# Performance work log

Hardware: AMD Instinct MI355X
Metric: run time of the kernel (lower is better)

## Reference

```python
import jax, jax.numpy as jnp
import numpy as np


def _conv(x, w, b, pad):
    # NCHW conv, stride 1, symmetric padding, torch Conv2d semantics (bias included)
    y = jax.lax.conv_general_dilated(x, w, (1, 1), [(pad, pad), (pad, pad)],
                                     dimension_numbers=('NCHW', 'OIHW', 'NCHW'))
    return y + b[None, :, None, None]


def _inorm(x, eps=1e-5):
    # torch nn.InstanceNorm2d default: affine=False, biased variance over (H, W)
    m = jnp.mean(x, axis=(2, 3), keepdims=True)
    v = jnp.var(x, axis=(2, 3), keepdims=True)
    return (x - m) * jax.lax.rsqrt(v + eps)


def _convT2x(x, wt):
    # torch ConvTranspose2d(k=3, stride=2, padding=1, output_padding=1, bias=False)
    # wt has torch layout (C_in, C_out, kH, kW); express as dilated conv with flipped kernel.
    # output size = 2*H exactly: pad low = k-1-p = 1, pad high = k-1-p+output_padding = 2.
    w = jnp.transpose(jnp.flip(wt, (2, 3)), (1, 0, 2, 3))  # -> (C_out, C_in, kH, kW)
    return jax.lax.conv_general_dilated(x, w, (1, 1), [(1, 2), (1, 2)],
                                        lhs_dilation=(2, 2),
                                        dimension_numbers=('NCHW', 'OIHW', 'NCHW'))


def setup_inputs() -> dict:
    key = jax.random.key(0)
    ks = jax.random.split(key, 24)
    B, C = 2, 256          # dim_list[0] = 256
    H4, W4 = 160, 240      # 1/4-scale feature map of a 640x960 image

    def n(k, shape, s=1.0):
        return jax.random.normal(k, shape, dtype=jnp.float32) * s

    return {
        # mono feature pyramid: 1/4, 1/8, 1/16, 1/32 scale, all C=dim_list[0]
        'f4':  n(ks[0], (B, C, H4, W4)),
        'f8':  n(ks[1], (B, C, H4 // 2, W4 // 2)),
        'f16': n(ks[2], (B, C, H4 // 4, W4 // 4)),
        'f32': n(ks[3], (B, C, H4 // 8, W4 // 8)),
        'w32': n(ks[4], (160, C, 3, 3), 0.02), 'b32': n(ks[5], (160,), 0.02),
        'wt32': n(ks[6], (160, 192, 3, 3), 0.02),
        'w16': n(ks[7], (192, 192 + C, 5, 5), 0.02), 'b16': n(ks[8], (192,), 0.02),
        'wr16': n(ks[9], (192, C, 1, 1), 0.02), 'br16': n(ks[10], (192,), 0.02),
        'wt16': n(ks[11], (192, 64, 3, 3), 0.02),
        'w8': n(ks[12], (64, 64 + C, 5, 5), 0.02), 'b8': n(ks[13], (64,), 0.02),
        'wr8': n(ks[14], (64, C, 1, 1), 0.02), 'br8': n(ks[15], (64,), 0.02),
        'wt8': n(ks[16], (64, 48, 3, 3), 0.02),
        'w4': n(ks[17], (48, 48 + C, 5, 5), 0.02), 'b4': n(ks[18], (48,), 0.02),
        'wr4': n(ks[19], (48, C, 1, 1), 0.02), 'br4': n(ks[20], (48,), 0.02),
    }


def reference(f4, f8, f16, f32, w32, b32, wt32, w16, b16, wr16, br16, wt16,
              w8, b8, wr8, br8, wt8, w4, b4, wr4, br4):
    # Feat_transfer.forward: coarse-to-fine fusion with residual 1x1 projections
    feat32 = jax.nn.relu(_inorm(_conv(f32, w32, b32, 1)))                 # [B,160,H/32,W/32]
    up32 = _convT2x(feat32, wt32)                                          # [B,192,H/16,W/16]
    feat16 = jax.nn.relu(_inorm(_conv(jnp.concatenate([f16, up32], 1), w16, b16, 2))) \
             + _conv(f16, wr16, br16, 0)                                   # [B,192,H/16,W/16]
    up16 = _convT2x(feat16, wt16)                                          # [B,64,H/8,W/8]
    feat8 = jax.nn.relu(_inorm(_conv(jnp.concatenate([f8, up16], 1), w8, b8, 2))) \
            + _conv(f8, wr8, br8, 0)                                       # [B,64,H/8,W/8]
    up8 = _convT2x(feat8, wt8)                                             # [B,48,H/4,W/4]
    feat4 = jax.nn.relu(_inorm(_conv(jnp.concatenate([f4, up8], 1), w4, b4, 2))) \
            + _conv(f4, wr4, br4, 0)                                       # [B,48,H/4,W/4]
    return (feat4, feat8, feat16, feat32)
```

## Files before the change

kernel.cpp:

```cpp
#include <hip/hip_runtime.h>
#include <hip/hip_bf16.h>

typedef __attribute__((ext_vector_type(8))) short bf16x8;
typedef __attribute__((ext_vector_type(4))) float f32x4;

static inline int cdiv(int a, int b) { return (a + b - 1) / b; }

__device__ __forceinline__ ushort f2bf(float f) {
    unsigned u = __float_as_uint(f);
    unsigned r = (u + 0x7FFFu + ((u >> 16) & 1u)) >> 16;
    return (ushort)r;
}
__device__ __forceinline__ unsigned pack2bf(float lo, float hi) {
    unsigned r;
    asm("v_cvt_pk_bf16_f32 %0, %1, %2" : "=v"(r) : "v"(lo), "v"(hi));
    return r;
}
__device__ __forceinline__ float bf2f(ushort u) {
    return __uint_as_float((unsigned)u << 16);
}

__global__ __launch_bounds__(256)
void transpose_w(const float* __restrict__ w, ushort* __restrict__ wt,
                 int Cout, int CoutPad, int Cin, int Cin_pad, int KK, int total) {
    int idx = blockIdx.x * 256 + threadIdx.x;
    if (idx >= total) return;
    int ci = idx % Cin_pad;
    int rem = idx / Cin_pad;
    int co = rem % CoutPad;
    int t  = rem / CoutPad;
    float v = (ci < Cin && co < Cout) ? w[((size_t)co * Cin + ci) * KK + t] : 0.f;
    wt[idx] = f2bf(v);
}

__device__ const int g_tky[9] = {1, 1, 1, 0, 2, 0, 0, 2, 2};
__device__ const int g_tkx[9] = {1, 0, 2, 1, 1, 0, 2, 0, 2};

__global__ __launch_bounds__(256)
void transpose_wt(const float* __restrict__ wt, ushort* __restrict__ dst,
                  int Cin, int Cout, int Cin_pad, int total) {
    int idx = blockIdx.x * 256 + threadIdx.x;
    if (idx >= total) return;
    int ci = idx % Cin_pad;
    int rem = idx / Cin_pad;
    int co = rem % Cout;
    int t  = rem / Cout;
    float v = 0.f;
    if (ci < Cin)
        v = wt[((size_t)(ci * Cout + co) * 3 + g_tky[t]) * 3 + g_tkx[t]];
    dst[idx] = f2bf(v);
}

template<int K, int TY, int TX, int NSPLIT, int MSPLIT, int MT, int OUTMODE>
__global__ __launch_bounds__(256)
void conv_mfma7(const float* __restrict__ in1, int C1,
                const ushort* __restrict__ in2, int C2, int Cin,
                const ushort* __restrict__ wt,
                void* __restrict__ outDst, size_t pStride,
                int H, int W, int Cout, int CoutPad, int Cin_pad,
                int tilesX, int tilesY, int nchunks, int cps) {
    constexpr int P = K / 2;
    constexpr int XOFF = (K == 1) ? 0 : 4;
    constexpr int JOFF = XOFF - P;
    constexpr int HXs = (TX + K - 1 + JOFF + 3) & ~3;
    constexpr int HY = TY + K - 1;
    constexpr int PITCH = 40;
    constexpr int KK = K * K;
    constexpr int PXW = TY * TX / NSPLIT;
    constexpr int NT = PXW / 16;
    constexpr int G = HXs / 4;
    constexpr int NITEM = 16 * HY * G;

    __shared__ ushort sT[HY * HXs * PITCH];

    const int tid = threadIdx.x;
    const int lane = tid & 63, wv = tid >> 6;
    const int nwave = wv % NSPLIT, mwave = wv / NSPLIT;
    const int l15 = lane & 15, lg = lane >> 4;

    const int nwg = tilesX * tilesY;
    int bid = blockIdx.x;
    int q8 = nwg >> 3, r8 = nwg & 7;
    int xcd = bid & 7, sidx = bid >> 3;
    int wg = (xcd < r8 ? xcd * (q8 + 1) : r8 * (q8 + 1) + (xcd - r8) * q8) + sidx;
    const int txi = wg / tilesY;
    const int tyi = wg % tilesY;

    const int b = blockIdx.z;
    const int x0 = txi * TX, y0 = tyi * TY;
    const size_t HW = (size_t)H * W;

    const int co0 = mwave * (MT * 16);

    int posBase[NT], py_[NT], px_[NT];
    #pragma unroll
    for (int nt = 0; nt < NT; ++nt) {
        int pidx = nwave * PXW + nt * 16 + l15;
        int py = pidx / TX, px = pidx % TX;
        py_[nt] = py; px_[nt] = px;
        posBase[nt] = (py * HXs + px + JOFF) * PITCH + lg * 8;
    }
    const int aoff = l15 * Cin_pad + lg * 8;

    f32x4 acc[MT][NT];
    #pragma unroll
    for (int i = 0; i < MT; ++i)
        #pragma unroll
        for (int j = 0; j < NT; ++j) acc[i][j] = (f32x4)0.f;

    const int c0 = blockIdx.y * cps;
    const int c1 = (c0 + cps < nchunks) ? c0 + cps : nchunks;

    for (int c = c0; c < c1; ++c) {
        const int ci0 = c * 32;
        __syncthreads();
        for (int i = tid; i < NITEM; i += 256) {
            int g  = i % G;
            int rr = (i / G) % HY;
            int cp = i / (G * HY);
            int ci = ci0 + cp * 2;
            int y  = y0 - P + rr;
            int xg = x0 - XOFF + g * 4;
            ushort* dp = &sT[(rr * HXs + g * 4) * PITCH + cp * 2];
            bool yok = (unsigned)y < (unsigned)H;
            unsigned d0, d1, d2, d3;
            if (ci < C1) {
                const float* p0 = in1 + (long long)(b * C1 + ci) * (long long)HW + (long long)y * W + xg;
                if (yok && xg >= 0 && (xg + 3) < W) {
                    float4 a  = *(const float4*)p0;
                    float4 b2 = *(const float4*)(p0 + HW);
                    d0 = pack2bf(a.x, b2.x);
                    d1 = pack2bf(a.y, b2.y);
                    d2 = pack2bf(a.z, b2.z);
                    d3 = pack2bf(a.w, b2.w);
                } else {
                    unsigned t0 = 0, t1 = 0, t2 = 0, t3 = 0;
                    #pragma unroll
                    for (int u = 0; u < 4; ++u) {
                        int x = xg + u;
                        unsigned pk = 0;
                        if (yok && (unsigned)x < (unsigned)W)
                            pk = (unsigned)f2bf(p0[u]) | ((unsigned)f2bf(p0[u + (long long)HW]) << 16);
                        if (u == 0) t0 = pk; else if (u == 1) t1 = pk;
                        else if (u == 2) t2 = pk; else t3 = pk;
                    }
                    d0 = t0; d1 = t1; d2 = t2; d3 = t3;
                }
            } else {
                const ushort* q0 = in2 + (long long)(b * C2 + (ci - C1)) * (long long)HW + (long long)y * W + xg;
                if (yok && xg >= 0 && (xg + 3) < W && (ci + 1) < Cin) {
                    ushort4 a  = *(const ushort4*)q0;
                    ushort4 b2 = *(const ushort4*)(q0 + HW);
                    d0 = (unsigned)a.x | ((unsigned)b2.x << 16);
                    d1 = (unsigned)a.y | ((unsigned)b2.y << 16);
                    d2 = (unsigned)a.z | ((unsigned)b2.z << 16);
                    d3 = (unsigned)a.w | ((unsigned)b2.w << 16);
                } else {
                    unsigned t0 = 0, t1 = 0, t2 = 0, t3 = 0;
                    #pragma unroll
                    for (int u = 0; u < 4; ++u) {
                        int x = xg + u;
                        unsigned pk = 0;
                        if (yok && (unsigned)x < (unsigned)W && ci < Cin) {
                            unsigned v0 = q0[u];
                            unsigned v1 = (ci + 1 < Cin) ? q0[u + (long long)HW] : 0u;
                            pk = v0 | (v1 << 16);
                        }
                        if (u == 0) t0 = pk; else if (u == 1) t1 = pk;
                        else if (u == 2) t2 = pk; else t3 = pk;
                    }
                    d0 = t0; d1 = t1; d2 = t2; d3 = t3;
                }
            }
            int s = (g + rr) & 3;
            #pragma unroll
            for (int u = 0; u < 4; ++u) {
                int cc2 = (u + s) & 3;
                unsigned val = (cc2 & 2) ? ((cc2 & 1) ? d3 : d2)
                                         : ((cc2 & 1) ? d1 : d0);
                *(unsigned*)(dp + cc2 * PITCH) = val;
            }
        }
        __syncthreads();

        bf16x8 af[4][MT];
        #pragma unroll
        for (int s = 0; s < 3; ++s) {
            if (s < KK) {
                const ushort* ap = wt + (size_t)((size_t)s * CoutPad + co0) * Cin_pad + ci0 + aoff;
                #pragma unroll
                for (int mt = 0; mt < MT; ++mt)
                    af[s][mt] = *(const bf16x8*)(ap + (size_t)mt * 16 * Cin_pad);
            }
        }
        #pragma unroll
        for (int t = 0; t < KK; ++t) {
            if (t + 3 < KK) {
                const ushort* ap = wt + (size_t)((size_t)(t + 3) * CoutPad + co0) * Cin_pad + ci0 + aoff;
                #pragma unroll
                for (int mt = 0; mt < MT; ++mt)
                    af[(t + 3) & 3][mt] = *(const bf16x8*)(ap + (size_t)mt * 16 * Cin_pad);
            }
            const int tOff = ((t / K) * HXs + (t % K)) * PITCH;
            bf16x8 bf[NT];
            #pragma unroll
            for (int nt = 0; nt < NT; ++nt)
                bf[nt] = *(const bf16x8*)(sT + posBase[nt] + tOff);
            #pragma unroll
            for (int mt = 0; mt < MT; ++mt)
                #pragma unroll
                for (int nt = 0; nt < NT; ++nt)
                    acc[mt][nt] = __builtin_amdgcn_mfma_f32_16x16x32_bf16(
                        af[t & 3][mt], bf[nt], acc[mt][nt], 0, 0, 0);
        }
    }

    float* baseF = (float*)outDst + (size_t)blockIdx.y * pStride;
    #pragma unroll
    for (int mt = 0; mt < MT; ++mt) {
        #pragma unroll
        for (int nt = 0; nt < NT; ++nt) {
            int y = y0 + py_[nt], x = x0 + px_[nt];
            if (y < H && x < W) {
                #pragma unroll
                for (int r = 0; r < 4; ++r) {
                    int co = co0 + mt * 16 + lg * 4 + r;
                    if (co < Cout) {
                        size_t o = ((size_t)(b * Cout + co)) * HW + (size_t)y * W + x;
                        if (OUTMODE == 0) baseF[o] = acc[mt][nt][r];
                        else              ((ushort*)outDst)[o] = f2bf(acc[mt][nt][r]);
                    }
                }
            }
        }
    }
}

template<int K, int TY, int TX, int NSPLIT, int MSPLIT, int MT>
__global__ __launch_bounds__(256)
void conv_mfma5(const float* __restrict__ in1, int C1, int Cin,
                const ushort* __restrict__ wt,
                float* __restrict__ outDst,
                int H, int W, int Cout, int CoutPad, int Cin_pad,
                int tilesX, int nchunks, int cps) {
    constexpr int P = K / 2;
    constexpr int XOFF = 4;
    constexpr int JOFF = XOFF - P;
    constexpr int HXs = (TX + K - 1 + JOFF + 3) & ~3;
    constexpr int HY = TY + K - 1;
    constexpr int PITCH = 40;
    constexpr int KK = K * K;
    constexpr int PXW = TY * TX / NSPLIT;
    constexpr int NT = PXW / 16;
    constexpr int G = HXs / 4;
    constexpr int NITEM = 16 * HY * G;

    __shared__ ushort sT[HY * HXs * PITCH];

    const int tid = threadIdx.x;
    const int lane = tid & 63, wv = tid >> 6;
    const int nwave = wv % NSPLIT, mwave = wv / NSPLIT;
    const int l15 = lane & 15, lg = lane >> 4;

    const int txi = blockIdx.x % tilesX;
    const int tyi = blockIdx.x / tilesX;
    const int b = blockIdx.z;
    const int x0 = txi * TX, y0 = tyi * TY;
    const size_t HW = (size_t)H * W;
    const int co0 = mwave * (MT * 16);

    int posBase[NT], py_[NT], px_[NT];
    #pragma unroll
    for (int nt = 0; nt < NT; ++nt) {
        int pidx = nwave * PXW + nt * 16 + l15;
        int py = pidx / TX, px = pidx % TX;
        py_[nt] = py; px_[nt] = px;
        posBase[nt] = (py * HXs + px + JOFF) * PITCH + lg * 8;
    }
    const int aoff = l15 * Cin_pad + lg * 8;

    f32x4 acc[MT][NT];
    #pragma unroll
    for (int i = 0; i < MT; ++i)
        #pragma unroll
        for (int j = 0; j < NT; ++j) acc[i][j] = (f32x4)0.f;

    const int c0 = blockIdx.y * cps;
    const int c1 = (c0 + cps < nchunks) ? c0 + cps : nchunks;

    for (int c = c0; c < c1; ++c) {
        const int ci0 = c * 32;
        __syncthreads();
        for (int i = tid; i < NITEM; i += 256) {
            int g  = i % G;
            int rr = (i / G) % HY;
            int cp = i / (G * HY);
            int ci = ci0 + cp * 2;
            int y  = y0 - P + rr;
            int xg = x0 - XOFF + g * 4;
            ushort* dp = &sT[(rr * HXs + g * 4) * PITCH + cp * 2];
            const float* p0 = in1 + (long long)(b * C1 + ci) * (long long)HW + (long long)y * W + xg;
            bool yok = (unsigned)y < (unsigned)H;
            #pragma unroll
            for (int u = 0; u < 4; ++u) {
                int x = xg + u;
                unsigned pk = 0;
                if (yok && (unsigned)x < (unsigned)W)
                    pk = (unsigned)f2bf(p0[u]) | ((unsigned)f2bf(p0[u + (long long)HW]) << 16);
                *(unsigned*)(dp + u * PITCH) = pk;
            }
        }
        __syncthreads();

        bf16x8 afA[MT];
        {
            const ushort* ap = wt + (size_t)co0 * Cin_pad + ci0 + aoff;
            #pragma unroll
            for (int mt = 0; mt < MT; ++mt)
                afA[mt] = *(const bf16x8*)(ap + (size_t)mt * 16 * Cin_pad);
        }
        #pragma unroll
        for (int t = 0; t < KK; ++t) {
            bf16x8 afB[MT];
            if (t + 1 < KK) {
                const ushort* ap = wt + (size_t)((t + 1) * CoutPad + co0) * Cin_pad + ci0 + aoff;
                #pragma unroll
                for (int mt = 0; mt < MT; ++mt)
                    afB[mt] = *(const bf16x8*)(ap + (size_t)mt * 16 * Cin_pad);
            }
            const int tOff = ((t / K) * HXs + (t % K)) * PITCH;
            bf16x8 bf[NT];
            #pragma unroll
            for (int nt = 0; nt < NT; ++nt)
                bf[nt] = *(const bf16x8*)(sT + posBase[nt] + tOff);
            #pragma unroll
            for (int mt = 0; mt < MT; ++mt)
                #pragma unroll
                for (int nt = 0; nt < NT; ++nt)
                    acc[mt][nt] = __builtin_amdgcn_mfma_f32_16x16x32_bf16(
                        afA[mt], bf[nt], acc[mt][nt], 0, 0, 0);
            if (t + 1 < KK) {
                #pragma unroll
                for (int mt = 0; mt < MT; ++mt) afA[mt] = afB[mt];
            }
        }
    }

    #pragma unroll
    for (int mt = 0; mt < MT; ++mt) {
        #pragma unroll
        for (int nt = 0; nt < NT; ++nt) {
            int y = y0 + py_[nt], x = x0 + px_[nt];
            if (y < H && x < W) {
                #pragma unroll
                for (int r = 0; r < 4; ++r) {
                    int co = co0 + mt * 16 + lg * 4 + r;
                    if (co < Cout) {
                        size_t o = ((size_t)(b * Cout + co)) * HW + (size_t)y * W + x;
                        unsafeAtomicAdd(&outDst[o], acc[mt][nt][r]);
                    }
                }
            }
        }
    }
}

template<int TY, int TX, int NSPLIT, int MT>
__global__ __launch_bounds__(256)
void convt_mfma(const float* __restrict__ in,
                const ushort* __restrict__ wtp,
                ushort* __restrict__ out,
                int Cin, int Cout, int Cin_pad, int Hin, int Win,
                int tilesX, int tilesY) {
    constexpr int HY = TY + 1, HX = TX + 1;
    constexpr int PITCH = 40;
    constexpr int NPX = TY * TX;
    constexpr int PXW = NPX / NSPLIT;
    constexpr int NT = PXW / 16;
    constexpr int NPOS = HY * HX;
    constexpr int NIT = (NPOS * 16 + 63) & ~63;

    __shared__ ushort sT[NPOS * PITCH];

    constexpr int toy[9] = {0, 0, 0, 1, 0, 1, 1, 0, 0};
    constexpr int tox[9] = {0, 1, 0, 0, 0, 1, 0, 1, 0};
    constexpr int tph[9] = {0, 1, 1, 2, 2, 3, 3, 3, 3};

    const int tid = threadIdx.x;
    const int lane = tid & 63, wv = tid >> 6;
    const int nwave = wv % NSPLIT, mwave = wv / NSPLIT;
    const int l15 = lane & 15, lg = lane >> 4;

    int tile = blockIdx.x;
    const int txi = tile % tilesX;
    int rem = tile / tilesX;
    const int tyi = rem % tilesY;
    const int b = rem / tilesY;
    const int x0 = txi * TX, y0 = tyi * TY;
    const size_t HWi = (size_t)Hin * Win;
    const int Wo = 2 * Win;
    const size_t HWo = (size_t)4 * HWi;

    const int co0 = mwave * (MT * 16);

    int posBase[NT], py_[NT], px_[NT];
    #pragma unroll
    for (int nt = 0; nt < NT; ++nt) {
        int pidx = nwave * PXW + nt * 16 + l15;
        int py = pidx / TX, px = pidx % TX;
        py_[nt] = py; px_[nt] = px;
        posBase[nt] = (py * HX + px) * PITCH + lg * 8;
    }
    const int aoff = l15 * Cin_pad + lg * 8;

    f32x4 acc[4][MT][NT];
    #pragma unroll
    for (int p = 0; p < 4; ++p)
        #pragma unroll
        for (int i = 0; i < MT; ++i)
            #pragma unroll
            for (int j = 0; j < NT; ++j) acc[p][i][j] = (f32x4)0.f;

    const int nchunks = Cin_pad / 32;
    for (int c = 0; c < nchunks; ++c) {
        const int ci0 = c * 32;
        __syncthreads();
        for (int i = tid; i < NIT; i += 256) {
            int cp = (i >> 2) & 15;
            int pos = (i & 3) | ((i >> 6) << 2);
            if (pos < NPOS) {
                int hy = pos / HX, hx = pos % HX;
                int y = y0 + hy, x = x0 + hx;
                int ci = ci0 + cp * 2;
                unsigned pk = 0;
                if ((unsigned)y < (unsigned)Hin && (unsigned)x < (unsigned)Win && ci < Cin) {
                    const float* p0 = in + (size_t)(b * Cin + ci) * HWi + (size_t)y * Win + x;
                    float v0 = p0[0];
                    float v1 = (ci + 1 < Cin) ? p0[HWi] : 0.f;
                    pk = pack2bf(v0, v1);
                }
                *(unsigned*)&sT[pos * PITCH + cp * 2] = pk;
            }
        }
        __syncthreads();

        bf16x8 afA[MT];
        {
            const ushort* ap = wtp + (size_t)co0 * Cin_pad + ci0 + aoff;
            #pragma unroll
            for (int mt = 0; mt < MT; ++mt)
                afA[mt] = *(const bf16x8*)(ap + (size_t)mt * 16 * Cin_pad);
        }
        #pragma unroll
        for (int t = 0; t < 9; ++t) {
            bf16x8 afB[MT];
            if (t + 1 < 9) {
                const ushort* ap = wtp + (size_t)((t + 1) * Cout + co0) * Cin_pad + ci0 + aoff;
                #pragma unroll
                for (int mt = 0; mt < MT; ++mt)
                    afB[mt] = *(const bf16x8*)(ap + (size_t)mt * 16 * Cin_pad);
            }
            const int tOff = (toy[t] * HX + tox[t]) * PITCH;
            bf16x8 bf[NT];
            #pragma unroll
            for (int nt = 0; nt < NT; ++nt)
                bf[nt] = *(const bf16x8*)(sT + posBase[nt] + tOff);
            #pragma unroll
            for (int mt = 0; mt < MT; ++mt)
                #pragma unroll
                for (int nt = 0; nt < NT; ++nt)
                    acc[tph[t]][mt][nt] = __builtin_amdgcn_mfma_f32_16x16x32_bf16(
                        afA[mt], bf[nt], acc[tph[t]][mt][nt], 0, 0, 0);
            if (t + 1 < 9) {
                #pragma unroll
                for (int mt = 0; mt < MT; ++mt) afA[mt] = afB[mt];
            }
        }
    }

    #pragma unroll
    for (int dy = 0; dy < 2; ++dy) {
        #pragma unroll
        for (int mt = 0; mt < MT; ++mt) {
            #pragma unroll
            for (int nt = 0; nt < NT; ++nt) {
                int y = y0 + py_[nt], x = x0 + px_[nt];
                if (y < Hin && x < Win) {
                    #pragma unroll
                    for (int r = 0; r < 4; ++r) {
                        int co = co0 + mt * 16 + lg * 4 + r;
                        unsigned pk = pack2bf(acc[dy * 2][mt][nt][r], acc[dy * 2 + 1][mt][nt][r]);
                        *(unsigned*)&out[((size_t)(b * Cout + co)) * HWo + (size_t)(2 * y + dy) * Wo + 2 * x] = pk;
                    }
                }
            }
        }
    }
}

__global__ __launch_bounds__(256)
void inorm_stats2(const float* __restrict__ x, size_t pStride, int NS,
                  float* __restrict__ mean, float* __restrict__ istd, int HW) {
    int bc = blockIdx.x;
    const float4* p = (const float4*)(x + (size_t)bc * HW);
    size_t st4 = pStride >> 2;
    int n4 = HW >> 2;
    float s = 0.f, ss = 0.f;
    for (int i = threadIdx.x; i < n4; i += 256) {
        float4 v = p[i];
        for (int sp = 1; sp < NS; ++sp) {
            float4 w = p[i + sp * st4];
            v.x += w.x; v.y += w.y; v.z += w.z; v.w += w.w;
        }
        s += v.x + v.y + v.z + v.w;
        ss += v.x * v.x + v.y * v.y + v.z * v.z + v.w * v.w;
    }
    #pragma unroll
    for (int o = 32; o > 0; o >>= 1) {
        s  += __shfl_down(s, o);
        ss += __shfl_down(ss, o);
    }
    __shared__ float sh[4][2];
    int wid = threadIdx.x >> 6, ln = threadIdx.x & 63;
    if (ln == 0) { sh[wid][0] = s; sh[wid][1] = ss; }
    __syncthreads();
    if (threadIdx.x == 0) {
        float S = 0.f, SS = 0.f;
        for (int i = 0; i < 4; ++i) { S += sh[i][0]; SS += sh[i][1]; }
        float m = S / HW;
        float v = SS / HW - m * m;
        v = v > 0.f ? v : 0.f;
        mean[bc] = m;
        istd[bc] = rsqrtf(v + 1e-5f);
    }
}

template<int RESMODE>
__global__ __launch_bounds__(256)
void epilogue2(const float* __restrict__ raw, size_t rawStride, int NS,
               const float* __restrict__ mean,
               const float* __restrict__ istd,
               const void* __restrict__ res, size_t resStride, int NSR,
               const float* __restrict__ br,
               float* __restrict__ feat,
               int HW, int Cout, int total4) {
    int i = blockIdx.x * 256 + threadIdx.x;
    if (i >= total4) return;
    int bc = (int)(((long long)i * 4) / HW);
    float m = mean[bc], is = istd[bc];
    size_t rs4 = rawStride >> 2;
    float4 r = ((const float4*)raw)[i];
    for (int sp = 1; sp < NS; ++sp) {
        float4 w = ((const float4*)raw)[i + sp * rs4];
        r.x += w.x; r.y += w.y; r.z += w.z; r.w += w.w;
    }
    float4 o;
    o.x = fmaxf((r.x - m) * is, 0.f);
    o.y = fmaxf((r.y - m) * is, 0.f);
    o.z = fmaxf((r.z - m) * is, 0.f);
    o.w = fmaxf((r.w - m) * is, 0.f);
    if (RESMODE == 1) {
        float bb = br[bc % Cout];
        size_t es4 = resStride >> 2;
        float4 e = ((const float4*)res)[i];
        for (int sp = 1; sp < NSR; ++sp) {
            float4 w = ((const float4*)res)[i + sp * es4];
            e.x += w.x; e.y += w.y; e.z += w.z; e.w += w.w;
        }
        o.x += e.x + bb; o.y += e.y + bb; o.z += e.z + bb; o.w += e.w + bb;
    } else if (RESMODE == 2) {
        float bb = br[bc % Cout];
        ushort4 e = ((const ushort4*)res)[i];
        o.x += bf2f(e.x) + bb; o.y += bf2f(e.y) + bb;
        o.z += bf2f(e.z) + bb; o.w += bf2f(e.w) + bb;
    }
    ((float4*)feat)[i] = o;
}

extern "C" void kernel_launch(void* const* d_in, const int* in_sizes, int n_in,
                              void* d_out, int out_size, void* d_ws, size_t ws_size,
                              hipStream_t stream) {
    const float* f4   = (const float*)d_in[0];
    const float* f8   = (const float*)d_in[1];
    const float* f16  = (const float*)d_in[2];
    const float* f32  = (const float*)d_in[3];
    const float* w32  = (const float*)d_in[4];
    const float* wt32 = (const float*)d_in[6];
    const float* w16  = (const float*)d_in[7];
    const float* wr16 = (const float*)d_in[9];
    const float* br16 = (const float*)d_in[10];
    const float* wt16 = (const float*)d_in[11];
    const float* w8   = (const float*)d_in[12];
    const float* wr8  = (const float*)d_in[14];
    const float* br8  = (const float*)d_in[15];
    const float* wt8  = (const float*)d_in[16];
    const float* w4   = (const float*)d_in[17];
    const float* wr4  = (const float*)d_in[19];
    const float* br4  = (const float*)d_in[20];

    float* out = (float*)d_out;

    const int B = 2, C = 256;
    const int H4 = 160, W4 = 240;
    const int H8 = 80,  W8 = 120;
    const int H16 = 40, W16 = 60;
    const int H32 = 20, W32 = 30;

    float* feat4  = out;
    float* feat8  = out + (size_t)B * 48 * H4 * W4;
    float* feat16 = feat8 + (size_t)B * 64 * H8 * W8;
    float* feat32 = feat16 + (size_t)B * 192 * H16 * W16;

    const size_t bufElems = (size_t)B * 48 * H4 * W4;
    ushort* wsUpB  = (ushort*)d_ws;
    float*  wsRawP = (float*)(wsUpB + bufElems);
    ushort* wsResB = (ushort*)(wsRawP + bufElems);
    float*  stMean = (float*)(wsResB + bufElems);
    float*  stIstd = stMean + 512;
    float*  wsResF = (float*)wsResB;

    ushort* wb = (ushort*)feat4;
    ushort* W32p = wb;
    ushort* W16p = W32p + 9 * 192 * 256;
    ushort* W8p  = W16p + 25 * 192 * 448;
    ushort* W4p  = W8p  + 25 * 64 * 320;
    ushort* R16p = W4p  + 25 * 64 * 320;
    ushort* R8p  = R16p + 192 * 256;
    ushort* R4p  = R8p  + 64 * 256;
    ushort* T32p = R4p  + 64 * 256;
    ushort* T16p = T32p + 9 * 192 * 160;
    ushort* T8p  = T16p + 9 * 64 * 192;

    {
        int t1 = 9 * 192 * 256;
        transpose_w<<<cdiv(t1, 256), 256, 0, stream>>>(w32, W32p, 160, 192, 256, 256, 9, t1);
        int t2 = 25 * 192 * 448;
        transpose_w<<<cdiv(t2, 256), 256, 0, stream>>>(w16, W16p, 192, 192, 448, 448, 25, t2);
        int t3 = 25 * 64 * 320;
        transpose_w<<<cdiv(t3, 256), 256, 0, stream>>>(w8, W8p, 64, 64, 320, 320, 25, t3);
        int t4 = 25 * 64 * 320;
        transpose_w<<<cdiv(t4, 256), 256, 0, stream>>>(w4, W4p, 48, 64, 304, 320, 25, t4);
        int t5 = 192 * 256;
        transpose_w<<<cdiv(t5, 256), 256, 0, stream>>>(wr16, R16p, 192, 192, 256, 256, 1, t5);
        int t6 = 64 * 256;
        transpose_w<<<cdiv(t6, 256), 256, 0, stream>>>(wr8, R8p, 64, 64, 256, 256, 1, t6);
        int t7 = 64 * 256;
        transpose_w<<<cdiv(t7, 256), 256, 0, stream>>>(wr4, R4p, 48, 64, 256, 256, 1, t7);
        int u1 = 9 * 192 * 160;
        transpose_wt<<<cdiv(u1, 256), 256, 0, stream>>>(wt32, T32p, 160, 192, 160, u1);
        int u2 = 9 * 64 * 192;
        transpose_wt<<<cdiv(u2, 256), 256, 0, stream>>>(wt16, T16p, 192, 64, 192, u2);
        int u3 = 9 * 48 * 64;
        transpose_wt<<<cdiv(u3, 256), 256, 0, stream>>>(wt8, T8p, 64, 48, 64, u3);
    }

    {
        hipMemsetAsync(wsRawP, 0, (size_t)B * 160 * H32 * W32 * 4, stream);
        int tX = cdiv(W32, 8), tY = cdiv(H32, 4);
        dim3 g(tX * tY, 8, B);
        conv_mfma5<3, 4, 8, 1, 4, 3><<<g, 256, 0, stream>>>(
            f32, C, C, W32p, wsRawP, H32, W32, 160, 192, 256, tX, 8, 1);
        inorm_stats2<<<B * 160, 256, 0, stream>>>(wsRawP, 0, 1, stMean, stIstd, H32 * W32);
        int tot4 = B * 160 * H32 * W32 / 4;
        epilogue2<0><<<cdiv(tot4, 256), 256, 0, stream>>>(
            wsRawP, 0, 1, stMean, stIstd, nullptr, 0, 0, nullptr, feat32, H32 * W32, 160, tot4);
        int uX = cdiv(W32, 8), uY = cdiv(H32, 2);
        convt_mfma<2, 8, 1, 3><<<uX * uY * B, 256, 0, stream>>>(
            feat32, T32p, wsUpB, 160, 192, 160, H32, W32, uX, uY);
    }
    {
        size_t SZ16 = (size_t)B * 192 * H16 * W16;
        int tX = cdiv(W16, 8), tY = cdiv(H16, 8);
        dim3 g(tX * tY, 4, B);
        conv_mfma7<5, 8, 8, 1, 4, 3, 0><<<g, 256, 0, stream>>>(
            f16, C, wsUpB, 192, 448, W16p, wsRawP, SZ16,
            H16, W16, 192, 192, 448, tX, tY, 14, 4);
        dim3 gr(tX * tY, 2, B);
        conv_mfma7<1, 8, 8, 1, 4, 3, 0><<<gr, 256, 0, stream>>>(
            f16, C, nullptr, 0, C, R16p, wsResF, SZ16,
            H16, W16, 192, 192, 256, tX, tY, 8, 4);
        inorm_stats2<<<B * 192, 256, 0, stream>>>(wsRawP, SZ16, 4, stMean, stIstd, H16 * W16);
        int tot4 = (int)(SZ16 / 4);
        epilogue2<1><<<cdiv(tot4, 256), 256, 0, stream>>>(
            wsRawP, SZ16, 4, stMean, stIstd, wsResF, SZ16, 2, br16, feat16, H16 * W16, 192, tot4);
        int uX = cdiv(W16, 8), uY = cdiv(H16, 4);
        convt_mfma<4, 8, 2, 2><<<uX * uY * B, 256, 0, stream>>>(
            feat16, T16p, wsUpB, 192, 64, 192, H16, W16, uX, uY);
    }
    {
        size_t SZ8 = (size_t)B * 64 * H8 * W8;
        int tX = cdiv(W8, 16), tY = cdiv(H8, 8);
        dim3 g(tX * tY, 3, B);
        conv_mfma7<5, 8, 16, 2, 2, 2, 0><<<g, 256, 0, stream>>>(
            f8, C, wsUpB, 64, 320, W8p, wsRawP, SZ8,
            H8, W8, 64, 64, 320, tX, tY, 10, 4);
        dim3 gr(tX * cdiv(H8, 4), 1, B);
        conv_mfma7<1, 4, 16, 1, 4, 1, 0><<<gr, 256, 0, stream>>>(
            f8, C, nullptr, 0, C, R8p, wsResF, SZ8,
            H8, W8, 64, 64, 256, tX, cdiv(H8, 4), 8, 8);
        inorm_stats2<<<B * 64, 256, 0, stream>>>(wsRawP, SZ8, 3, stMean, stIstd, H8 * W8);
        int tot4 = (int)(SZ8 / 4);
        epilogue2<1><<<cdiv(tot4, 256), 256, 0, stream>>>(
            wsRawP, SZ8, 3, stMean, stIstd, wsResF, SZ8, 1, br8, feat8, H8 * W8, 64, tot4);
        int uX = cdiv(W8, 16), uY = cdiv(H8, 4);
        convt_mfma<4, 16, 4, 3><<<uX * uY * B, 256, 0, stream>>>(
            feat8, T8p, wsUpB, 64, 48, 64, H8, W8, uX, uY);
    }
    {
        size_t SZ4 = (size_t)B * 48 * H4 * W4;
        int tX = cdiv(W4, 16), tY = cdiv(H4, 8);
        dim3 g(tX * tY, 1, B);
        conv_mfma7<5, 8, 16, 2, 2, 2, 0><<<g, 256, 0, stream>>>(
            f4, C, wsUpB, 48, 304, W4p, wsRawP, SZ4,
            H4, W4, 48, 64, 320, tX, tY, 10, 10);
        conv_mfma7<1, 8, 16, 2, 2, 2, 2><<<g, 256, 0, stream>>>(
            f4, C, nullptr, 0, C, R4p, wsResB, 0,
            H4, W4, 48, 64, 256, tX, tY, 8, 8);
        inorm_stats2<<<B * 48, 256, 0, stream>>>(wsRawP, 0, 1, stMean, stIstd, H4 * W4);
        int tot4 = (int)(SZ4 / 4);
        epilogue2<2><<<cdiv(tot4, 256), 256, 0, stream>>>(
            wsRawP, 0, 1, stMean, stIstd, wsResB, 0, 0, br4, feat4, H4 * W4, 48, tot4);
    }
}
```

Before: 594.1 us.

## Raise split-K for 5x5 convs and store bf16 partial sums

The 5x5 fusion convs now split the input-channel reduction across more blocks (7, 5 and 2 splits instead of 4, 3 and 1), and the 1/16 conv uses smaller spatial tiles. To keep the extra partial buffers cheap, each split writes its partial sums as bf16 instead of fp32. New stats and epilogue kernels read and sum the bf16 partials. This adds parallelism and occupancy for the small-resolution convs and cuts partial-sum traffic, at the cost of bf16 rounding on every partial before the instance norm and more partial buffers to read back.

```diff
diff --git a/kernel.cpp b/kernel.cpp
--- a/kernel.cpp
+++ b/kernel.cpp
@@ -215,7 +215,8 @@
         }
     }
 
-    float* baseF = (float*)outDst + (size_t)blockIdx.y * pStride;
+    float*  baseF = (float*)outDst + (size_t)blockIdx.y * pStride;
+    ushort* baseU = (ushort*)outDst + (size_t)blockIdx.y * pStride;
     #pragma unroll
     for (int mt = 0; mt < MT; ++mt) {
         #pragma unroll
@@ -228,7 +229,7 @@
                     if (co < Cout) {
                         size_t o = ((size_t)(b * Cout + co)) * HW + (size_t)y * W + x;
                         if (OUTMODE == 0) baseF[o] = acc[mt][nt][r];
-                        else              ((ushort*)outDst)[o] = f2bf(acc[mt][nt][r]);
+                        else              baseU[o] = f2bf(acc[mt][nt][r]);
                     }
                 }
             }
@@ -535,9 +536,64 @@
     }
 }
 
+__global__ __launch_bounds__(256)
+void inorm_statsB(const ushort* __restrict__ x, size_t pStride, int NS,
+                  float* __restrict__ mean, float* __restrict__ istd, int HW) {
+    int bc = blockIdx.x;
+    const ushort* base = x + (size_t)bc * HW;
+    int n4 = HW >> 2;
+    float s = 0.f, ss = 0.f;
+    for (int i = threadIdx.x; i < n4; i += 256) {
+        float v0 = 0.f, v1 = 0.f, v2 = 0.f, v3 = 0.f;
+        for (int sp = 0; sp < NS; ++sp) {
+            ushort4 u = *(const ushort4*)(base + sp * pStride + (size_t)i * 4);
+            v0 += bf2f(u.x); v1 += bf2f(u.y); v2 += bf2f(u.z); v3 += bf2f(u.w);
+        }
+        s += v0 + v1 + v2 + v3;
+        ss += v0 * v0 + v1 * v1 + v2 * v2 + v3 * v3;
+    }
+    #pragma unroll
+    for (int o = 32; o > 0; o >>= 1) {
+        s  += __shfl_down(s, o);
+        ss += __shfl_down(ss, o);
+    }
+    __shared__ float sh[4][2];
+    int wid = threadIdx.x >> 6, ln = threadIdx.x & 63;
+    if (ln == 0) { sh[wid][0] = s; sh[wid][1] = ss; }
+    __syncthreads();
+    if (threadIdx.x == 0) {
+        float S = 0.f, SS = 0.f;
+        for (int i = 0; i < 4; ++i) { S += sh[i][0]; SS += sh[i][1]; }
+        float m = S / HW;
+        float v = SS / HW - m * m;
+        v = v > 0.f ? v : 0.f;
+        mean[bc] = m;
+        istd[bc] = rsqrtf(v + 1e-5f);
+    }
+}
+
+__global__ __launch_bounds__(256)
+void epilogue2(const float* __restrict__ raw,
+               const float* __restrict__ mean,
+               const float* __restrict__ istd,
+               float* __restrict__ feat,
+               int HW, int total4) {
+    int i = blockIdx.x * 256 + threadIdx.x;
+    if (i >= total4) return;
+    int bc = (int)(((long long)i * 4) / HW);
+    float m = mean[bc], is = istd[bc];
+    float4 r = ((const float4*)raw)[i];
+    float4 o;
+    o.x = fmaxf((r.x - m) * is, 0.f);
+    o.y = fmaxf((r.y - m) * is, 0.f);
+    o.z = fmaxf((r.z - m) * is, 0.f);
+    o.w = fmaxf((r.w - m) * is, 0.f);
+    ((float4*)feat)[i] = o;
+}
+
 template<int RESMODE>
 __global__ __launch_bounds__(256)
-void epilogue2(const float* __restrict__ raw, size_t rawStride, int NS,
+void epilogueB(const ushort* __restrict__ rawB, size_t rawStride, int NS,
                const float* __restrict__ mean,
                const float* __restrict__ istd,
                const void* __restrict__ res, size_t resStride, int NSR,
@@ -548,19 +604,18 @@
     if (i >= total4) return;
     int bc = (int)(((long long)i * 4) / HW);
     float m = mean[bc], is = istd[bc];
-    size_t rs4 = rawStride >> 2;
-    float4 r = ((const float4*)raw)[i];
-    for (int sp = 1; sp < NS; ++sp) {
-        float4 w = ((const float4*)raw)[i + sp * rs4];
-        r.x += w.x; r.y += w.y; r.z += w.z; r.w += w.w;
+    float r0 = 0.f, r1 = 0.f, r2 = 0.f, r3 = 0.f;
+    for (int sp = 0; sp < NS; ++sp) {
+        ushort4 u = *(const ushort4*)(rawB + sp * rawStride + (size_t)i * 4);
+        r0 += bf2f(u.x); r1 += bf2f(u.y); r2 += bf2f(u.z); r3 += bf2f(u.w);
     }
     float4 o;
-    o.x = fmaxf((r.x - m) * is, 0.f);
-    o.y = fmaxf((r.y - m) * is, 0.f);
-    o.z = fmaxf((r.z - m) * is, 0.f);
-    o.w = fmaxf((r.w - m) * is, 0.f);
+    o.x = fmaxf((r0 - m) * is, 0.f);
+    o.y = fmaxf((r1 - m) * is, 0.f);
+    o.z = fmaxf((r2 - m) * is, 0.f);
+    o.w = fmaxf((r3 - m) * is, 0.f);
+    float bb = br[bc % Cout];
     if (RESMODE == 1) {
-        float bb = br[bc % Cout];
         size_t es4 = resStride >> 2;
         float4 e = ((const float4*)res)[i];
         for (int sp = 1; sp < NSR; ++sp) {
@@ -568,8 +623,7 @@
             e.x += w.x; e.y += w.y; e.z += w.z; e.w += w.w;
         }
         o.x += e.x + bb; o.y += e.y + bb; o.z += e.z + bb; o.w += e.w + bb;
-    } else if (RESMODE == 2) {
-        float bb = br[bc % Cout];
+    } else {
         ushort4 e = ((const ushort4*)res)[i];
         o.x += bf2f(e.x) + bb; o.y += bf2f(e.y) + bb;
         o.z += bf2f(e.z) + bb; o.w += bf2f(e.w) + bb;
@@ -613,11 +667,12 @@
 
     const size_t bufElems = (size_t)B * 48 * H4 * W4;
     ushort* wsUpB  = (ushort*)d_ws;
-    float*  wsRawP = (float*)(wsUpB + bufElems);
-    ushort* wsResB = (ushort*)(wsRawP + bufElems);
+    ushort* wsRawB = (ushort*)(wsUpB + bufElems);
+    ushort* wsResB = (ushort*)(wsRawB + 2 * bufElems);
     float*  stMean = (float*)(wsResB + bufElems);
     float*  stIstd = stMean + 512;
     float*  wsResF = (float*)wsResB;
+    float*  wsRawF = (float*)wsRawB;
 
     ushort* wb = (ushort*)feat4;
     ushort* W32p = wb;
@@ -655,34 +710,34 @@
     }
 
     {
-        hipMemsetAsync(wsRawP, 0, (size_t)B * 160 * H32 * W32 * 4, stream);
+        hipMemsetAsync(wsRawF, 0, (size_t)B * 160 * H32 * W32 * 4, stream);
         int tX = cdiv(W32, 8), tY = cdiv(H32, 4);
         dim3 g(tX * tY, 8, B);
         conv_mfma5<3, 4, 8, 1, 4, 3><<<g, 256, 0, stream>>>(
-            f32, C, C, W32p, wsRawP, H32, W32, 160, 192, 256, tX, 8, 1);
-        inorm_stats2<<<B * 160, 256, 0, stream>>>(wsRawP, 0, 1, stMean, stIstd, H32 * W32);
+            f32, C, C, W32p, wsRawF, H32, W32, 160, 192, 256, tX, 8, 1);
+        inorm_stats2<<<B * 160, 256, 0, stream>>>(wsRawF, 0, 1, stMean, stIstd, H32 * W32);
         int tot4 = B * 160 * H32 * W32 / 4;
-        epilogue2<0><<<cdiv(tot4, 256), 256, 0, stream>>>(
-            wsRawP, 0, 1, stMean, stIstd, nullptr, 0, 0, nullptr, feat32, H32 * W32, 160, tot4);
+        epilogue2<<<cdiv(tot4, 256), 256, 0, stream>>>(
+            wsRawF, stMean, stIstd, feat32, H32 * W32, tot4);
         int uX = cdiv(W32, 8), uY = cdiv(H32, 2);
         convt_mfma<2, 8, 1, 3><<<uX * uY * B, 256, 0, stream>>>(
             feat32, T32p, wsUpB, 160, 192, 160, H32, W32, uX, uY);
     }
     {
         size_t SZ16 = (size_t)B * 192 * H16 * W16;
-        int tX = cdiv(W16, 8), tY = cdiv(H16, 8);
-        dim3 g(tX * tY, 4, B);
-        conv_mfma7<5, 8, 8, 1, 4, 3, 0><<<g, 256, 0, stream>>>(
-            f16, C, wsUpB, 192, 448, W16p, wsRawP, SZ16,
-            H16, W16, 192, 192, 448, tX, tY, 14, 4);
+        int tX = cdiv(W16, 8), tY = cdiv(H16, 4);
+        dim3 g(tX * tY, 7, B);
+        conv_mfma7<5, 4, 8, 1, 4, 3, 2><<<g, 256, 0, stream>>>(
+            f16, C, wsUpB, 192, 448, W16p, wsRawB, SZ16,
+            H16, W16, 192, 192, 448, tX, tY, 14, 2);
         dim3 gr(tX * tY, 2, B);
-        conv_mfma7<1, 8, 8, 1, 4, 3, 0><<<gr, 256, 0, stream>>>(
+        conv_mfma7<1, 4, 8, 1, 4, 3, 0><<<gr, 256, 0, stream>>>(
             f16, C, nullptr, 0, C, R16p, wsResF, SZ16,
             H16, W16, 192, 192, 256, tX, tY, 8, 4);
-        inorm_stats2<<<B * 192, 256, 0, stream>>>(wsRawP, SZ16, 4, stMean, stIstd, H16 * W16);
+        inorm_statsB<<<B * 192, 256, 0, stream>>>(wsRawB, SZ16, 7, stMean, stIstd, H16 * W16);
         int tot4 = (int)(SZ16 / 4);
-        epilogue2<1><<<cdiv(tot4, 256), 256, 0, stream>>>(
-            wsRawP, SZ16, 4, stMean, stIstd, wsResF, SZ16, 2, br16, feat16, H16 * W16, 192, tot4);
+        epilogueB<1><<<cdiv(tot4, 256), 256, 0, stream>>>(
+            wsRawB, SZ16, 7, stMean, stIstd, wsResF, SZ16, 2, br16, feat16, H16 * W16, 192, tot4);
         int uX = cdiv(W16, 8), uY = cdiv(H16, 4);
         convt_mfma<4, 8, 2, 2><<<uX * uY * B, 256, 0, stream>>>(
             feat16, T16p, wsUpB, 192, 64, 192, H16, W16, uX, uY);
@@ -690,18 +745,18 @@
     {
         size_t SZ8 = (size_t)B * 64 * H8 * W8;
         int tX = cdiv(W8, 16), tY = cdiv(H8, 8);
-        dim3 g(tX * tY, 3, B);
-        conv_mfma7<5, 8, 16, 2, 2, 2, 0><<<g, 256, 0, stream>>>(
-            f8, C, wsUpB, 64, 320, W8p, wsRawP, SZ8,
-            H8, W8, 64, 64, 320, tX, tY, 10, 4);
+        dim3 g(tX * tY, 5, B);
+        conv_mfma7<5, 8, 16, 2, 2, 2, 2><<<g, 256, 0, stream>>>(
+            f8, C, wsUpB, 64, 320, W8p, wsRawB, SZ8,
+            H8, W8, 64, 64, 320, tX, tY, 10, 2);
         dim3 gr(tX * cdiv(H8, 4), 1, B);
         conv_mfma7<1, 4, 16, 1, 4, 1, 0><<<gr, 256, 0, stream>>>(
             f8, C, nullptr, 0, C, R8p, wsResF, SZ8,
             H8, W8, 64, 64, 256, tX, cdiv(H8, 4), 8, 8);
-        inorm_stats2<<<B * 64, 256, 0, stream>>>(wsRawP, SZ8, 3, stMean, stIstd, H8 * W8);
+        inorm_statsB<<<B * 64, 256, 0, stream>>>(wsRawB, SZ8, 5, stMean, stIstd, H8 * W8);
         int tot4 = (int)(SZ8 / 4);
-        epilogue2<1><<<cdiv(tot4, 256), 256, 0, stream>>>(
-            wsRawP, SZ8, 3, stMean, stIstd, wsResF, SZ8, 1, br8, feat8, H8 * W8, 64, tot4);
+        epilogueB<1><<<cdiv(tot4, 256), 256, 0, stream>>>(
+            wsRawB, SZ8, 5, stMean, stIstd, wsResF, SZ8, 1, br8, feat8, H8 * W8, 64, tot4);
         int uX = cdiv(W8, 16), uY = cdiv(H8, 4);
         convt_mfma<4, 16, 4, 3><<<uX * uY * B, 256, 0, stream>>>(
             feat8, T8p, wsUpB, 64, 48, 64, H8, W8, uX, uY);
@@ -709,16 +764,17 @@
     {
         size_t SZ4 = (size_t)B * 48 * H4 * W4;
         int tX = cdiv(W4, 16), tY = cdiv(H4, 8);
-        dim3 g(tX * tY, 1, B);
-        conv_mfma7<5, 8, 16, 2, 2, 2, 0><<<g, 256, 0, stream>>>(
-            f4, C, wsUpB, 48, 304, W4p, wsRawP, SZ4,
-            H4, W4, 48, 64, 320, tX, tY, 10, 10);
-        conv_mfma7<1, 8, 16, 2, 2, 2, 2><<<g, 256, 0, stream>>>(
+        dim3 g(tX * tY, 2, B);
+        conv_mfma7<5, 8, 16, 2, 2, 2, 2><<<g, 256, 0, stream>>>(
+            f4, C, wsUpB, 48, 304, W4p, wsRawB, SZ4,
+            H4, W4, 48, 64, 320, tX, tY, 10, 5);
+        dim3 gr(tX * tY, 1, B);
+        conv_mfma7<1, 8, 16, 2, 2, 2, 2><<<gr, 256, 0, stream>>>(
             f4, C, nullptr, 0, C, R4p, wsResB, 0,
             H4, W4, 48, 64, 256, tX, tY, 8, 8);
-        inorm_stats2<<<B * 48, 256, 0, stream>>>(wsRawP, 0, 1, stMean, stIstd, H4 * W4);
+        inorm_statsB<<<B * 48, 256, 0, stream>>>(wsRawB, SZ4, 2, stMean, stIstd, H4 * W4);
         int tot4 = (int)(SZ4 / 4);
-        epilogue2<2><<<cdiv(tot4, 256), 256, 0, stream>>>(
-            wsRawP, 0, 1, stMean, stIstd, wsResB, 0, 0, br4, feat4, H4 * W4, 48, tot4);
-    }
-}
+        epilogueB<2><<<cdiv(tot4, 256), 256, 0, stream>>>(
+            wsRawB, SZ4, 2, stMean, stIstd, wsResB, 0, 0, br4, feat4, H4 * W4, 48, tot4);
+    }
+}
```

New measurement: 642.1 us. +8.1%, slower.
